# Kernel optimization log

Hardware: AMD Instinct MI355X
Metric: run time of the kernel (lower is better)

The kernel has to match this reference:

```python
import jax, jax.numpy as jnp
import numpy as np

N = 200000   # number of nodes / adj columns
F = 256      # input_features
L0 = 256     # layers[0]
L1 = 128     # layers[1]


def setup_inputs() -> dict:
    key = jax.random.key(0)
    k_adj, k_feat, k0, kb0, k1, kb1, ks = jax.random.split(key, 7)
    adj = jax.random.randint(k_adj, (1, N), 0, 2, dtype=jnp.int32)
    feature = jax.random.normal(k_feat, (N, F), dtype=jnp.float32)
    # MLP params: Linear(2F, L0) -> relu -> Linear(L0, L1) -> relu; score Linear(L1, 1, bias=False)
    W0 = jax.random.normal(k0, (2 * F, L0), dtype=jnp.float32) * 0.02
    b0 = jax.random.normal(kb0, (L0,), dtype=jnp.float32) * 0.02
    W1 = jax.random.normal(k1, (L0, L1), dtype=jnp.float32) * 0.02
    b1 = jax.random.normal(kb1, (L1,), dtype=jnp.float32) * 0.02
    w_score = jax.random.normal(ks, (L1, 1), dtype=jnp.float32) * 0.02
    return {"adj": adj, "feature": feature, "W0": W0, "b0": b0,
            "W1": W1, "b1": b1, "w_score": w_score}


def reference(adj, feature, W0, b0, W1, b1, w_score):
    # Original forward only processes row i=0 of adj (loop breaks immediately).
    # idx = nonzero columns of adj[0], plus sentinel -233 at the end.
    # Neighbor feature is feature[v] if v > 0 else zeros (so column 0 and the
    # sentinel both get a zero vector). Softmax is over the neighbor set (dim 0);
    # we realize this as a masked softmax over all N columns + 1 sentinel slot.
    n, f = feature.shape
    row = adj[0]
    mask = jnp.concatenate([row != 0, jnp.ones((1,), dtype=bool)])  # [n+1]
    # neighbor features: feature[v] for v=0..n-1 (v=0 -> zeros), plus zero sentinel row
    neigh = jnp.concatenate([feature.at[0].set(0.0),
                             jnp.zeros((1, f), feature.dtype)], axis=0)  # [n+1, f]
    self_feat = jnp.broadcast_to(feature[0], (n + 1, f))                 # [n+1, f]
    s = jnp.concatenate([self_feat, neigh], axis=1)                      # [n+1, 2f]
    h = jax.nn.relu(s @ W0 + b0)                                         # [n+1, L0]
    h = jax.nn.relu(h @ W1 + b1)                                         # [n+1, L1]
    scores = h @ w_score                                                 # [n+1, 1]
    scores = jnp.where(mask[:, None], scores, jnp.float32(-1e30))
    lk = jax.nn.softmax(scores, axis=0)
    return jnp.where(mask[:, None], lk, 0.0)
```

## Files before the change

kernel.cpp:

```cpp
#include <hip/hip_runtime.h>
#include <stdint.h>

#define NN   200000
#define NTOT 200001

typedef short bf16x8 __attribute__((ext_vector_type(8)));
typedef float f32x16 __attribute__((ext_vector_type(16)));

union FragU { bf16x8 v; unsigned q[4]; };

__device__ __forceinline__ unsigned bfrne(float x) {
  unsigned u = __float_as_uint(x);
  return (u + 0x7fffu + ((u >> 16) & 1u)) >> 16;
}
__device__ __forceinline__ unsigned pk2(float a, float b) {
  return bfrne(a) | (bfrne(b) << 16);
}

__global__ void gnn_prep(const int* __restrict__ adj, const float* __restrict__ feat,
                         const float* __restrict__ W0, const float* __restrict__ b0,
                         const float* __restrict__ W1, const float* __restrict__ b1,
                         const float* __restrict__ wsc, float* __restrict__ c0g,
                         char* __restrict__ w0t, char* __restrict__ w1t,
                         float* __restrict__ scores, float* __restrict__ S,
                         int* __restrict__ cnt)
{
  const int tid = threadIdx.x;
  if (blockIdx.x == 0) {
    __shared__ float h0z[256];
    __shared__ float h1z[128];
    float a = b0[tid];
    for (int f = 0; f < 256; ++f) a = fmaf(feat[f], W0[f * 256 + tid], a);
    c0g[tid] = a;
    h0z[tid] = fmaxf(a, 0.f);
    __syncthreads();
    if (tid < 128) {
      float t = b1[tid];
      for (int k = 0; k < 256; ++k) t = fmaf(h0z[k], W1[k * 128 + tid], t);
      h1z[tid] = fmaxf(t, 0.f) * wsc[tid];
    }
    __syncthreads();
    if (tid == 0) {
      float sz = 0.f;
      for (int p = 0; p < 128; ++p) sz += h1z[p];
      scores[0]  = sz;
      scores[NN] = sz;
      *S = expf(sz) * (adj[0] != 0 ? 2.f : 1.f);
      *cnt = 0;
    }
  } else {
    int gid = (blockIdx.x - 1) * 256 + tid;
    if (gid < 8192) {
      int m = gid >> 5, a = gid & 31, k0 = a * 8;
      unsigned q0 = pk2(W0[(256 + k0 + 0) * 256 + m], W0[(256 + k0 + 1) * 256 + m]);
      unsigned q1 = pk2(W0[(256 + k0 + 2) * 256 + m], W0[(256 + k0 + 3) * 256 + m]);
      unsigned q2 = pk2(W0[(256 + k0 + 4) * 256 + m], W0[(256 + k0 + 5) * 256 + m]);
      unsigned q3 = pk2(W0[(256 + k0 + 6) * 256 + m], W0[(256 + k0 + 7) * 256 + m]);
      *(uint4*)(w0t + m * 512 + ((a ^ (m & 7)) << 4)) = make_uint4(q0, q1, q2, q3);
    } else if (gid < 12288) {
      int g2 = gid - 8192;
      int p = g2 >> 5, a = g2 & 31;
      int base = 32 * (a >> 2) + 16 * ((a >> 1) & 1) + 4 * (a & 1);
      unsigned q0 = pk2(W1[(base + 0)  * 128 + p], W1[(base + 1)  * 128 + p]);
      unsigned q1 = pk2(W1[(base + 2)  * 128 + p], W1[(base + 3)  * 128 + p]);
      unsigned q2 = pk2(W1[(base + 8)  * 128 + p], W1[(base + 9)  * 128 + p]);
      unsigned q3 = pk2(W1[(base + 10) * 128 + p], W1[(base + 11) * 128 + p]);
      *(uint4*)(w1t + p * 512 + ((a ^ (p & 7)) << 4)) = make_uint4(q0, q1, q2, q3);
    }
  }
}

__global__ __launch_bounds__(1024) void
gnn_compact(const int* __restrict__ adj, int* __restrict__ idx, int* __restrict__ cnt)
{
  __shared__ int wc[64];
  __shared__ int bbase;
  const int tid  = threadIdx.x;
  const int wave = tid >> 6, lane = tid & 63;
  const int R = blockIdx.x * 4096;

  unsigned long long mk[4];
#pragma unroll
  for (int p = 0; p < 4; ++p) {
    int i = R + p * 1024 + tid;
    bool f = (i > 0) && (i < NN) && (adj[i] != 0);
    mk[p] = __ballot(f);
  }
  if (lane == 0) {
#pragma unroll
    for (int p = 0; p < 4; ++p) wc[p * 16 + wave] = __popcll(mk[p]);
  }
  __syncthreads();
  if (tid == 0) {
    int run = 0;
    for (int e = 0; e < 64; ++e) { int v = wc[e]; wc[e] = run; run += v; }
    bbase = atomicAdd(cnt, run);
  }
  __syncthreads();
  const int b0 = bbase;
#pragma unroll
  for (int p = 0; p < 4; ++p) {
    if ((mk[p] >> lane) & 1ull) {
      int i = R + p * 1024 + tid;
      idx[b0 + wc[p * 16 + wave] + __popcll(mk[p] & ((1ull << lane) - 1ull))] = i;
    }
  }
}

__global__ __launch_bounds__(256, 2) void
gnn_main(const float* __restrict__ feat, const char* __restrict__ w0t,
         const char* __restrict__ w1t, const float* __restrict__ c0g,
         const float* __restrict__ b1, const float* __restrict__ wsc,
         const int* __restrict__ idx, const int* __restrict__ cnt,
         float* __restrict__ scores, float* __restrict__ S)
{
  __shared__ __align__(16) char sW[2][32768];
  __shared__ float c0s[256];
  __shared__ float b1s[128];
  __shared__ float wss[128];
  __shared__ float wsum[4];

  const int M = *cnt;
  if ((int)blockIdx.x * 128 >= M) return;

  const int tid  = threadIdx.x;
  const int wave = tid >> 6, lane = tid & 63;
  const int h = lane >> 5, nl = lane & 31;

  const int slot = blockIdx.x * 128 + wave * 32 + nl;
  const int node = idx[min(slot, M - 1)];

  auto stage = [&](int buf, const char* gsrc) {
    const char* gp = gsrc + (wave << 13) + (lane << 4);
    char* lp = &sW[buf][wave << 13];
#pragma unroll
    for (int i = 0; i < 8; ++i)
      __builtin_amdgcn_global_load_lds(
          (const __attribute__((address_space(1))) unsigned*)(gp + (i << 10)),
          (__attribute__((address_space(3))) unsigned*)(lp + (i << 10)),
          16, 0, 0);
  };

  stage(0, w0t);

  FragU fB[16];
  const float4* frow = (const float4*)(feat + (size_t)node * 256);
#pragma unroll
  for (int kk = 0; kk < 16; ++kk) {
    float4 x = frow[4 * kk + 2 * h];
    float4 y = frow[4 * kk + 2 * h + 1];
    fB[kk].q[0] = pk2(x.x, x.y);
    fB[kk].q[1] = pk2(x.z, x.w);
    fB[kk].q[2] = pk2(y.x, y.y);
    fB[kk].q[3] = pk2(y.z, y.w);
  }

  c0s[tid] = c0g[tid];
  if (tid < 128) { b1s[tid] = b1[tid]; wss[tid] = wsc[tid]; }
  __syncthreads();

  unsigned h0p[8][8];
#pragma unroll
  for (int c = 0; c < 4; ++c) {
    stage((c + 1) & 1, (c < 3) ? (w0t + (c + 1) * 32768) : w1t);
    const char* Bp = sW[c & 1];
    f32x16 acc0, acc1;
#pragma unroll
    for (int i = 0; i < 16; ++i) { acc0[i] = 0.f; acc1[i] = 0.f; }
#pragma unroll
    for (int kk = 0; kk < 16; ++kk) {
      bf16x8 a0 = *(const bf16x8*)(Bp + nl * 512        + (((2 * kk + h) ^ (nl & 7)) << 4));
      bf16x8 a1 = *(const bf16x8*)(Bp + (32 + nl) * 512 + (((2 * kk + h) ^ (nl & 7)) << 4));
      acc0 = __builtin_amdgcn_mfma_f32_32x32x16_bf16(a0, fB[kk].v, acc0, 0, 0, 0);
      acc1 = __builtin_amdgcn_mfma_f32_32x32x16_bf16(a1, fB[kk].v, acc1, 0, 0, 0);
    }
#pragma unroll
    for (int t = 0; t < 2; ++t) {
      const f32x16& ac = t ? acc1 : acc0;
      const int tile = c * 2 + t, nb = tile * 32;
#pragma unroll
      for (int g = 0; g < 4; ++g) {
        float4 cv = *(const float4*)&c0s[nb + 8 * g + 4 * h];
        float v0 = fmaxf(ac[4 * g + 0] + cv.x, 0.f);
        float v1 = fmaxf(ac[4 * g + 1] + cv.y, 0.f);
        float v2 = fmaxf(ac[4 * g + 2] + cv.z, 0.f);
        float v3 = fmaxf(ac[4 * g + 3] + cv.w, 0.f);
        h0p[tile][2 * g + 0] = pk2(v0, v1);
        h0p[tile][2 * g + 1] = pk2(v2, v3);
      }
    }
    __syncthreads();
  }

  f32x16 acc2[4];
#pragma unroll
  for (int t = 0; t < 4; ++t)
#pragma unroll
    for (int i = 0; i < 16; ++i) acc2[t][i] = 0.f;

#pragma unroll
  for (int c2 = 0; c2 < 2; ++c2) {
    if (c2 == 0) stage(1, w1t + 32768);
    const char* Bp = sW[c2];
#pragma unroll
    for (int kk = 0; kk < 16; ++kk) {
      bf16x8 a0 = *(const bf16x8*)(Bp + nl * 512        + (((2 * kk + h) ^ (nl & 7)) << 4));
      bf16x8 a1 = *(const bf16x8*)(Bp + (32 + nl) * 512 + (((2 * kk + h) ^ (nl & 7)) << 4));
      FragU bb;
      const int tt = kk >> 1, p = kk & 1;
      bb.q[0] = h0p[tt][4 * p + 0];
      bb.q[1] = h0p[tt][4 * p + 1];
      bb.q[2] = h0p[tt][4 * p + 2];
      bb.q[3] = h0p[tt][4 * p + 3];
      acc2[c2 * 2 + 0] = __builtin_amdgcn_mfma_f32_32x32x16_bf16(a0, bb.v, acc2[c2 * 2 + 0], 0, 0, 0);
      acc2[c2 * 2 + 1] = __builtin_amdgcn_mfma_f32_32x32x16_bf16(a1, bb.v, acc2[c2 * 2 + 1], 0, 0, 0);
    }
    if (c2 == 0) __syncthreads();
  }

  float sc = 0.f;
#pragma unroll
  for (int pt = 0; pt < 4; ++pt) {
#pragma unroll
    for (int g = 0; g < 4; ++g) {
      float4 bv = *(const float4*)&b1s[pt * 32 + 8 * g + 4 * h];
      float4 wv = *(const float4*)&wss[pt * 32 + 8 * g + 4 * h];
      sc += fmaxf(acc2[pt][4 * g + 0] + bv.x, 0.f) * wv.x;
      sc += fmaxf(acc2[pt][4 * g + 1] + bv.y, 0.f) * wv.y;
      sc += fmaxf(acc2[pt][4 * g + 2] + bv.z, 0.f) * wv.z;
      sc += fmaxf(acc2[pt][4 * g + 3] + bv.w, 0.f) * wv.w;
    }
  }
  sc += __shfl_xor(sc, 32, 64);
  if (h == 0 && slot < M) scores[node] = sc;

  float ex = (slot < M) ? expf(sc) : 0.f;
#pragma unroll
  for (int off = 32; off; off >>= 1) ex += __shfl_xor(ex, off, 64);
  if (lane == 0) wsum[wave] = ex * 0.5f;
  __syncthreads();
  if (tid == 0) atomicAdd(S, wsum[0] + wsum[1] + wsum[2] + wsum[3]);
}

__global__ void gnn_final(const int* __restrict__ adj, const float* __restrict__ scores,
                          const float* __restrict__ S, float* __restrict__ out)
{
  int i = blockIdx.x * blockDim.x + threadIdx.x;
  if (i > NN) return;
  bool m = (i == NN) || (adj[i] != 0);
  float Sv = *S;
  out[i] = m ? expf(scores[i]) / Sv : 0.f;
}

extern "C" void kernel_launch(void* const* d_in, const int* in_sizes, int n_in,
                              void* d_out, int out_size, void* d_ws, size_t ws_size,
                              hipStream_t stream)
{
  (void)in_sizes; (void)n_in; (void)out_size; (void)ws_size;
  const int*   adj  = (const int*)d_in[0];
  const float* feat = (const float*)d_in[1];
  const float* W0   = (const float*)d_in[2];
  const float* b0   = (const float*)d_in[3];
  const float* W1   = (const float*)d_in[4];
  const float* b1   = (const float*)d_in[5];
  const float* wsc  = (const float*)d_in[6];
  float* out = (float*)d_out;

  char* ws = (char*)d_ws;
  float* scores = (float*)ws;
  char*  w0t    = ws + 800256;
  char*  w1t    = ws + 931328;
  float* c0g    = (float*)(ws + 996864);
  float* S      = (float*)(ws + 997888);
  int*   cnt    = (int*)(ws + 997904);
  int*   idxb   = (int*)(ws + 997952);

  gnn_prep   <<<49,   256,  0, stream>>>(adj, feat, W0, b0, W1, b1, wsc, c0g, w0t, w1t, scores, S, cnt);
  gnn_compact<<<49,   1024, 0, stream>>>(adj, idxb, cnt);
  gnn_main   <<<1563, 256,  0, stream>>>(feat, w0t, w1t, c0g, b1, wsc, idxb, cnt, scores, S);
  gnn_final  <<<782,  256,  0, stream>>>(adj, scores, S, out);
}
```

Baseline: 321.7 us.

## Fuse compaction into prep kernel and replace score atomics with per-block partials

The adjacency compaction pass now runs as extra blocks inside the prep kernel, which removes one kernel launch; the counter is zeroed with a memset issued beforehand. The main kernel writes a per-block partial exp-sum instead of doing an atomicAdd on a single global value. Every block of the final kernel re-reduces all 1563 partials before normalising. This trades launch overhead and atomic contention for redundant partial reductions in each final block and an extra memset.

```diff
diff --git a/kernel.cpp b/kernel.cpp
--- a/kernel.cpp
+++ b/kernel.cpp
@@ -1,8 +1,9 @@
 #include <hip/hip_runtime.h>
 #include <stdint.h>
 
-#define NN   200000
-#define NTOT 200001
+#define NN    200000
+#define NTOT  200001
+#define NPART 1563
 
 typedef short bf16x8 __attribute__((ext_vector_type(8)));
 typedef float f32x16 __attribute__((ext_vector_type(16)));
@@ -23,7 +24,7 @@
                          const float* __restrict__ wsc, float* __restrict__ c0g,
                          char* __restrict__ w0t, char* __restrict__ w1t,
                          float* __restrict__ scores, float* __restrict__ S,
-                         int* __restrict__ cnt)
+                         int* __restrict__ idx, int* __restrict__ cnt)
 {
   const int tid = threadIdx.x;
   if (blockIdx.x == 0) {
@@ -46,9 +47,8 @@
       scores[0]  = sz;
       scores[NN] = sz;
       *S = expf(sz) * (adj[0] != 0 ? 2.f : 1.f);
-      *cnt = 0;
-    }
-  } else {
+    }
+  } else if (blockIdx.x < 49) {
     int gid = (blockIdx.x - 1) * 256 + tid;
     if (gid < 8192) {
       int m = gid >> 5, a = gid & 31, k0 = a * 8;
@@ -67,42 +67,34 @@
       unsigned q3 = pk2(W1[(base + 10) * 128 + p], W1[(base + 11) * 128 + p]);
       *(uint4*)(w1t + p * 512 + ((a ^ (p & 7)) << 4)) = make_uint4(q0, q1, q2, q3);
     }
-  }
-}
-
-__global__ __launch_bounds__(1024) void
-gnn_compact(const int* __restrict__ adj, int* __restrict__ idx, int* __restrict__ cnt)
-{
-  __shared__ int wc[64];
-  __shared__ int bbase;
-  const int tid  = threadIdx.x;
-  const int wave = tid >> 6, lane = tid & 63;
-  const int R = blockIdx.x * 4096;
-
-  unsigned long long mk[4];
-#pragma unroll
-  for (int p = 0; p < 4; ++p) {
-    int i = R + p * 1024 + tid;
-    bool f = (i > 0) && (i < NN) && (adj[i] != 0);
-    mk[p] = __ballot(f);
-  }
-  if (lane == 0) {
-#pragma unroll
-    for (int p = 0; p < 4; ++p) wc[p * 16 + wave] = __popcll(mk[p]);
-  }
-  __syncthreads();
-  if (tid == 0) {
-    int run = 0;
-    for (int e = 0; e < 64; ++e) { int v = wc[e]; wc[e] = run; run += v; }
-    bbase = atomicAdd(cnt, run);
-  }
-  __syncthreads();
-  const int b0 = bbase;
-#pragma unroll
-  for (int p = 0; p < 4; ++p) {
-    if ((mk[p] >> lane) & 1ull) {
-      int i = R + p * 1024 + tid;
-      idx[b0 + wc[p * 16 + wave] + __popcll(mk[p] & ((1ull << lane) - 1ull))] = i;
+  } else {
+    __shared__ int wc[64];
+    __shared__ int bbase;
+    const int wave = tid >> 6, lane = tid & 63;
+    const int R = (blockIdx.x - 49) * 4096;
+
+    unsigned long long mk[16];
+#pragma unroll
+    for (int p = 0; p < 16; ++p) {
+      int i = R + p * 256 + tid;
+      bool f = (i > 0) && (i < NN) && (adj[i] != 0);
+      mk[p] = __ballot(f);
+      if (lane == 0) wc[p * 4 + wave] = __popcll(mk[p]);
+    }
+    __syncthreads();
+    if (tid == 0) {
+      int run = 0;
+      for (int e = 0; e < 64; ++e) { int v = wc[e]; wc[e] = run; run += v; }
+      bbase = atomicAdd(cnt, run);
+    }
+    __syncthreads();
+    const int bb = bbase;
+#pragma unroll
+    for (int p = 0; p < 16; ++p) {
+      if ((mk[p] >> lane) & 1ull) {
+        int i = R + p * 256 + tid;
+        idx[bb + wc[p * 4 + wave] + __popcll(mk[p] & ((1ull << lane) - 1ull))] = i;
+      }
     }
   }
 }
@@ -112,7 +104,7 @@
          const char* __restrict__ w1t, const float* __restrict__ c0g,
          const float* __restrict__ b1, const float* __restrict__ wsc,
          const int* __restrict__ idx, const int* __restrict__ cnt,
-         float* __restrict__ scores, float* __restrict__ S)
+         float* __restrict__ scores, float* __restrict__ partial)
 {
   __shared__ __align__(16) char sW[2][32768];
   __shared__ float c0s[256];
@@ -120,10 +112,13 @@
   __shared__ float wss[128];
   __shared__ float wsum[4];
 
+  const int tid = threadIdx.x;
   const int M = *cnt;
-  if ((int)blockIdx.x * 128 >= M) return;
-
-  const int tid  = threadIdx.x;
+  if ((int)blockIdx.x * 128 >= M) {
+    if (tid == 0) partial[blockIdx.x] = 0.f;
+    return;
+  }
+
   const int wave = tid >> 6, lane = tid & 63;
   const int h = lane >> 5, nl = lane & 31;
 
@@ -239,16 +234,29 @@
   for (int off = 32; off; off >>= 1) ex += __shfl_xor(ex, off, 64);
   if (lane == 0) wsum[wave] = ex * 0.5f;
   __syncthreads();
-  if (tid == 0) atomicAdd(S, wsum[0] + wsum[1] + wsum[2] + wsum[3]);
+  if (tid == 0) partial[blockIdx.x] = wsum[0] + wsum[1] + wsum[2] + wsum[3];
 }
 
 __global__ void gnn_final(const int* __restrict__ adj, const float* __restrict__ scores,
-                          const float* __restrict__ S, float* __restrict__ out)
-{
-  int i = blockIdx.x * blockDim.x + threadIdx.x;
+                          const float* __restrict__ S, const float* __restrict__ partial,
+                          float* __restrict__ out)
+{
+  __shared__ float red[4];
+  __shared__ float Svs;
+  const int tid = threadIdx.x;
+  float loc = 0.f;
+  for (int j = tid; j < NPART; j += 256) loc += partial[j];
+#pragma unroll
+  for (int off = 32; off; off >>= 1) loc += __shfl_xor(loc, off, 64);
+  if ((tid & 63) == 0) red[tid >> 6] = loc;
+  __syncthreads();
+  if (tid == 0) Svs = *S + red[0] + red[1] + red[2] + red[3];
+  __syncthreads();
+  const float Sv = Svs;
+
+  int i = blockIdx.x * 256 + tid;
   if (i > NN) return;
   bool m = (i == NN) || (adj[i] != 0);
-  float Sv = *S;
   out[i] = m ? expf(scores[i]) / Sv : 0.f;
 }
 
@@ -267,16 +275,17 @@
   float* out = (float*)d_out;
 
   char* ws = (char*)d_ws;
-  float* scores = (float*)ws;
-  char*  w0t    = ws + 800256;
-  char*  w1t    = ws + 931328;
-  float* c0g    = (float*)(ws + 996864);
-  float* S      = (float*)(ws + 997888);
-  int*   cnt    = (int*)(ws + 997904);
-  int*   idxb   = (int*)(ws + 997952);
-
-  gnn_prep   <<<49,   256,  0, stream>>>(adj, feat, W0, b0, W1, b1, wsc, c0g, w0t, w1t, scores, S, cnt);
-  gnn_compact<<<49,   1024, 0, stream>>>(adj, idxb, cnt);
-  gnn_main   <<<1563, 256,  0, stream>>>(feat, w0t, w1t, c0g, b1, wsc, idxb, cnt, scores, S);
-  gnn_final  <<<782,  256,  0, stream>>>(adj, scores, S, out);
-}
+  float* scores  = (float*)ws;
+  char*  w0t     = ws + 800256;
+  char*  w1t     = ws + 931328;
+  float* c0g     = (float*)(ws + 996864);
+  float* S       = (float*)(ws + 997888);
+  int*   cnt     = (int*)(ws + 997904);
+  int*   idxb    = (int*)(ws + 997952);
+  float* partial = (float*)(ws + 1797952);
+
+  hipMemsetAsync(cnt, 0, 4, stream);
+  gnn_prep <<<98,    256, 0, stream>>>(adj, feat, W0, b0, W1, b1, wsc, c0g, w0t, w1t, scores, S, idxb, cnt);
+  gnn_main <<<NPART, 256, 0, stream>>>(feat, w0t, w1t, c0g, b1, wsc, idxb, cnt, scores, partial);
+  gnn_final<<<782,   256, 0, stream>>>(adj, scores, S, partial, out);
+}
```

Result: no change. 317.9 us (-1.2%).
